# Performance work log

Hardware: AMD Instinct MI355X
Metric: run time of the kernel (lower is better)

## Reference

```python
import jax, jax.numpy as jnp
import numpy as np

GAMMA = 2.0
ALPHA = 0.25
NEG_TH = 0.4
POS_TH = 0.5
NUM_CLASSES = 80
STRIDES = [8, 16, 32, 64, 128]
IMG_H, IMG_W = 800, 1024
LEVEL_HW = [(100, 128), (50, 64), (25, 32), (13, 16), (7, 8)]


def _base_anchors(stride):
    # standard RetinaNet: octave_base_scale=4, 3 scales/octave, ratios 0.5/1/2
    scales = 4.0 * stride * np.array([2 ** 0, 2 ** (1.0 / 3), 2 ** (2.0 / 3)])
    ratios = np.array([0.5, 1.0, 2.0])
    h_r = np.sqrt(ratios)
    w_r = 1.0 / h_r
    ws = (w_r[:, None] * scales[None, :]).reshape(-1)
    hs = (h_r[:, None] * scales[None, :]).reshape(-1)
    return np.stack([-ws / 2, -hs / 2, ws / 2, hs / 2], axis=1)  # [9,4]


def build_anchors():
    out = []
    for (h, w), s in zip(LEVEL_HW, STRIDES):
        base = _base_anchors(s)
        xs = (np.arange(w) + 0.5) * s
        ys = (np.arange(h) + 0.5) * s
        cx, cy = np.meshgrid(xs, ys)  # [h,w]
        ctr = np.stack([cx, cy, cx, cy], axis=-1)  # [h,w,4]
        a = ctr[:, :, None, :] + base[None, None, :, :]  # [h,w,9,4] anchor-fastest
        out.append(a.reshape(-1, 4))
    return jnp.asarray(np.concatenate(out, axis=0), dtype=jnp.float32)  # [A,4]


def _iou(gt, an):  # [G,4],[A,4] -> [G,A]
    lt = jnp.maximum(gt[:, None, :2], an[None, :, :2])
    rb = jnp.minimum(gt[:, None, 2:], an[None, :, 2:])
    wh = jnp.clip(rb - lt, 0.0)
    inter = wh[..., 0] * wh[..., 1]
    area_g = (gt[:, 2] - gt[:, 0]) * (gt[:, 3] - gt[:, 1])
    area_a = (an[:, 2] - an[:, 0]) * (an[:, 3] - an[:, 1])
    return inter / (area_g[:, None] + area_a[None, :] - inter + 1e-6)


def _encode(an, gt):  # delta encoding, mean=0 std=1
    aw = an[:, 2] - an[:, 0]
    ah = an[:, 3] - an[:, 1]
    ax = (an[:, 0] + an[:, 2]) * 0.5
    ay = (an[:, 1] + an[:, 3]) * 0.5
    gw = gt[:, 2] - gt[:, 0]
    gh = gt[:, 3] - gt[:, 1]
    gx = (gt[:, 0] + gt[:, 2]) * 0.5
    gy = (gt[:, 1] + gt[:, 3]) * 0.5
    return jnp.stack([(gx - ax) / aw, (gy - ay) / ah, jnp.log(gw / aw), jnp.log(gh / ah)], axis=1)


def _per_image(logits, regp, gtb, gtl, anchors):
    G = gtb.shape[0]
    iou = _iou(gtb, anchors)  # [G,A]
    max_ov = iou.max(axis=0)
    arg_ov = iou.argmax(axis=0)
    assigned = jnp.where(max_ov < NEG_TH, 0, -1)
    assigned = jnp.where(max_ov >= POS_TH, arg_ov + 1, assigned)
    max_gt = iou.max(axis=1)
    eq = iou == max_gt[:, None]
    any_eq = eq.any(axis=0)
    last_j = (G - 1) - jnp.argmax(eq[::-1], axis=0)
    assigned = jnp.where(any_eq, last_j + 1, assigned)
    pos = assigned > 0
    neg = assigned == 0
    gi = jnp.clip(assigned - 1, 0, G - 1)
    labels = jnp.where(pos, gtl[gi], NUM_CLASSES)  # negatives get label = num_classes
    include = (pos | neg).astype(logits.dtype)  # ignored anchors contribute 0
    # focal loss
    p = jnp.clip(jax.nn.sigmoid(logits), 1e-6, 1.0 - 1e-6)
    cr = jnp.arange(NUM_CLASSES)[None, :]
    t = labels[:, None]
    term1 = (1.0 - p) ** GAMMA * jnp.log(p)
    term2 = p ** GAMMA * jnp.log(1.0 - p)
    per = -(t == cr).astype(p.dtype) * term1 * ALPHA - ((t != cr) & (t >= 0)).astype(p.dtype) * term2 * (1.0 - ALPHA)
    cls_sum = (per.sum(axis=1) * include).sum()
    # smooth-free L1 on positives
    reg_t = _encode(anchors, gtb[gi])
    reg_sum = (jnp.abs(regp - reg_t).sum(axis=1) * pos.astype(regp.dtype)).sum()
    return cls_sum, reg_sum, pos.sum()


def _flatten_levels(levels, c):
    n = levels[0].shape[0]
    return jnp.concatenate([p.transpose(0, 2, 3, 1).reshape(n, -1, c) for p in levels], axis=1)


def reference(cls_p0, cls_p1, cls_p2, cls_p3, cls_p4, reg_p0, reg_p1, reg_p2, reg_p3, reg_p4, gt_bboxes, gt_labels):
    anchors = build_anchors()
    cls = _flatten_levels([cls_p0, cls_p1, cls_p2, cls_p3, cls_p4], NUM_CLASSES)  # [N,A,80]
    reg = _flatten_levels([reg_p0, reg_p1, reg_p2, reg_p3, reg_p4], 4)  # [N,A,4]
    cls_s, reg_s, npos = jax.vmap(lambda l, r, b, t: _per_image(l, r, b, t, anchors))(cls, reg, gt_bboxes, gt_labels)
    num_pos = jnp.maximum(npos.sum(), 1).astype(cls.dtype)
    return (cls_s.sum() / num_pos, reg_s.sum() / num_pos)


def setup_inputs() -> dict:
    key = jax.random.key(0)
    ks = jax.random.split(key, 16)
    N, G = 2, 32
    d = {}
    for i, (h, w) in enumerate(LEVEL_HW):
        d[f"cls_p{i}"] = jax.random.normal(ks[i], (N, 9 * NUM_CLASSES, h, w), jnp.float32)
        d[f"reg_p{i}"] = jax.random.normal(ks[5 + i], (N, 9 * 4, h, w), jnp.float32)
    cx = jax.random.uniform(ks[10], (N, G), minval=50.0, maxval=IMG_W - 50.0)
    cy = jax.random.uniform(ks[11], (N, G), minval=50.0, maxval=IMG_H - 50.0)
    bw = jax.random.uniform(ks[12], (N, G), minval=32.0, maxval=300.0)
    bh = jax.random.uniform(ks[13], (N, G), minval=32.0, maxval=300.0)
    x1 = jnp.clip(cx - bw / 2, 0.0, IMG_W - 2.0)
    y1 = jnp.clip(cy - bh / 2, 0.0, IMG_H - 2.0)
    x2 = jnp.clip(cx + bw / 2, x1 + 1.0, float(IMG_W))
    y2 = jnp.clip(cy + bh / 2, y1 + 1.0, float(IMG_H))
    d["gt_bboxes"] = jnp.stack([x1, y1, x2, y2], axis=-1)
    d["gt_labels"] = jax.random.randint(ks[14], (N, G), 0, NUM_CLASSES)
    return d
```

## Files before the change

kernel.cpp:

```cpp
#include <hip/hip_runtime.h>
#include <stdint.h>

namespace {
constexpr int A_TOTAL = 153576;
constexpr int NG      = 32;
constexpr int NIMG    = 2;
constexpr int NCLS    = 80;
constexpr int NBLK_CLS = 2430;

constexpr size_t WS_CLS0  = 0;
constexpr size_t WS_REG   = 2048;
constexpr size_t WS_NPOS  = 4096;
constexpr size_t WS_MAXGT = 6144;
constexpr size_t WS_LABEL = 6656;
constexpr size_t WS_ZERO  = 6656;
}

__device__ __attribute__((noinline)) float4 anchor_box(int idx) {
    int base, lw, stride;
    if      (idx < 115200) { base = 0;      lw = 7; stride = 8;   }
    else if (idx < 144000) { base = 115200; lw = 6; stride = 16;  }
    else if (idx < 151200) { base = 144000; lw = 5; stride = 32;  }
    else if (idx < 153072) { base = 151200; lw = 4; stride = 64;  }
    else                   { base = 153072; lw = 3; stride = 128; }
    int s    = idx - base;
    int cell = s / 9;
    int a    = s - cell * 9;
    int y    = cell >> lw;
    int x    = cell - (y << lw);
    int r    = a / 3;
    int k    = a - r * 3;
    double c3 = (k == 0) ? 1.0 : ((k == 1) ? 1.2599210498948731648 : 1.5874010519681994748);
    double hr = (r == 0) ? 0.70710678118654752440 : ((r == 1) ? 1.0 : 1.4142135623730950488);
    double scale = 4.0 * (double)stride * c3;
    double wr  = 1.0 / hr;
    double wsz = wr * scale;
    double hsz = hr * scale;
    double cx  = ((double)x + 0.5) * (double)stride;
    double cy  = ((double)y + 0.5) * (double)stride;
    float4 out;
    out.x = (float)(cx - wsz / 2.0);
    out.y = (float)(cy - hsz / 2.0);
    out.z = (float)(cx + wsz / 2.0);
    out.w = (float)(cy + hsz / 2.0);
    return out;
}

__device__ __forceinline__ float iou_fn(float4 an, float4 g) {
#pragma clang fp contract(off)
    float ltx = fmaxf(g.x, an.x), lty = fmaxf(g.y, an.y);
    float rbx = fminf(g.z, an.z), rby = fminf(g.w, an.w);
    float w = fmaxf(rbx - ltx, 0.f), h = fmaxf(rby - lty, 0.f);
    float inter = w * h;
    float ag = (g.z - g.x) * (g.w - g.y);
    float aa = (an.z - an.x) * (an.w - an.y);
    return inter / (ag + aa - inter + 1e-6f);
}

__global__ __launch_bounds__(256)
void kmaxgt(const float* __restrict__ gtb, unsigned* __restrict__ maxgt) {
    int n   = blockIdx.y;
    int tid = threadIdx.x;
    int anchor = blockIdx.x * 128 + (tid >> 1);
    int half   = tid & 1;
    __shared__ float4   g_s[NG];
    __shared__ unsigned smax[NG];
    if (tid < NG) {
        g_s[tid]  = ((const float4*)gtb)[n * NG + tid];
        smax[tid] = 0u;
    }
    __syncthreads();
    bool  valid = anchor < A_TOTAL;
    float4 an = anchor_box(valid ? anchor : 0);
    int lane = tid & 63;
    for (int jj = 0; jj < 16; ++jj) {
        int j = half * 16 + jj;
        float iou = valid ? iou_fn(an, g_s[j]) : 0.f;
        for (int off = 2; off <= 32; off <<= 1)
            iou = fmaxf(iou, __shfl_xor(iou, off));
        if (lane < 2) atomicMax(&smax[j], __float_as_uint(iou));
    }
    __syncthreads();
    if (tid < NG) atomicMax(&maxgt[n * NG + tid], smax[tid]);
}

__global__ __launch_bounds__(256)
void kassign(const float* __restrict__ gtb, const int* __restrict__ gtl,
             const float* __restrict__ maxgt, uint8_t* __restrict__ labels,
             const float* __restrict__ r0, const float* __restrict__ r1,
             const float* __restrict__ r2, const float* __restrict__ r3,
             const float* __restrict__ r4,
             char* __restrict__ ws) {
    int n   = blockIdx.y;
    int tid = threadIdx.x;
    int anchor = blockIdx.x * 128 + (tid >> 1);
    int half   = tid & 1;
    __shared__ float4 g_s[NG];
    __shared__ float  mg_s[NG];
    __shared__ int    gl_s[NG];
    if (tid < NG) {
        g_s[tid]  = ((const float4*)gtb)[n * NG + tid];
        mg_s[tid] = maxgt[n * NG + tid];
        gl_s[tid] = gtl[n * NG + tid];
    }
    __syncthreads();
    bool  valid = anchor < A_TOTAL;
    float4 an = anchor_box(valid ? anchor : 0);
    float best = -1.f; int arg = 0; int last = -1;
    for (int jj = 0; jj < 16; ++jj) {
        int j = half * 16 + jj;
        float iou = iou_fn(an, g_s[j]);
        if (iou > best) { best = iou; arg = j; }
        if (iou == mg_s[j]) last = j;
    }
    float ob = __shfl_xor(best, 1);
    int   oa = __shfl_xor(arg, 1);
    int   ol = __shfl_xor(last, 1);
    if (ob > best) { best = ob; arg = oa; }
    if (ol > last) last = ol;
    int assigned = -1;
    if (best < 0.4f)  assigned = 0;
    if (best >= 0.5f) assigned = arg + 1;
    if (last >= 0)    assigned = last + 1;

    float rsum = 0.f; bool pos = false;
    if (valid && half == 0) {
        int base, HW; const float* rp;
        if      (anchor < 115200) { base = 0;      HW = 12800; rp = r0; }
        else if (anchor < 144000) { base = 115200; HW = 3200;  rp = r1; }
        else if (anchor < 151200) { base = 144000; HW = 800;   rp = r2; }
        else if (anchor < 153072) { base = 151200; HW = 208;   rp = r3; }
        else                      { base = 153072; HW = 56;    rp = r4; }
        int s = anchor - base;
        int cell = s / 9; int a = s - cell * 9;

        uint8_t lab;
        if (assigned > 0) {
            pos = true;
            int gi = assigned - 1;
            lab = (uint8_t)gl_s[gi];
            float aw = an.z - an.x, ah = an.w - an.y;
            float ax = (an.x + an.z) * 0.5f, ay = (an.y + an.w) * 0.5f;
            float4 g = g_s[gi];
            float gw = g.z - g.x, gh = g.w - g.y;
            float gx = (g.x + g.z) * 0.5f, gy = (g.y + g.w) * 0.5f;
            float t0 = (gx - ax) / aw, t1 = (gy - ay) / ah;
            float t2 = __logf(gw / aw), t3 = __logf(gh / ah);
            long off = (long)(n * 36 + a * 4) * HW + cell;
            float p0 = rp[off], p1 = rp[off + HW], p2 = rp[off + 2 * HW], p3 = rp[off + 3 * HW];
            rsum = fabsf(p0 - t0) + fabsf(p1 - t1) + fabsf(p2 - t2) + fabsf(p3 - t3);
        } else {
            lab = (assigned == 0) ? (uint8_t)NCLS : (uint8_t)255;
        }
        labels[n * A_TOTAL + base + a * HW + cell] = lab;
    }
    for (int off = 32; off; off >>= 1) rsum += __shfl_xor(rsum, off);
    unsigned long long bal = __ballot(pos);
    __shared__ float pr[4];
    __shared__ int   pn[4];
    int wid = tid >> 6;
    if ((tid & 63) == 0) { pr[wid] = rsum; pn[wid] = __popcll(bal); }
    __syncthreads();
    if (tid == 0) {
        float s = pr[0] + pr[1] + pr[2] + pr[3];
        int   c = pn[0] + pn[1] + pn[2] + pn[3];
        size_t slot = (size_t)(blockIdx.x & 7) * 256;
        atomicAdd((double*)(ws + WS_REG  + slot), (double)s);
        atomicAdd((int*)   (ws + WS_NPOS + slot), c);
    }
}

__device__ __forceinline__ float focal(float z, int c, int lab) {
    float e   = __expf(z);
    float u   = 1.f + e;
    float inv = __builtin_amdgcn_rcpf(u);
    float L   = __logf(u);
    float p   = e * inv;
    float t2  = 0.75f * (p * p) * L;
    float t1  = 0.25f * (inv * inv) * (L - z);
    float r   = (c == lab) ? t1 : t2;
    return (lab == 255) ? 0.f : r;
}

template <int HW, int BASE, int BPL>
__device__ float cls_level(const float* __restrict__ cp,
                           const uint8_t* __restrict__ labels, int rel, int lane) {
    int slab  = rel / (BPL * 4);
    int rem   = rel - slab * (BPL * 4);
    int chunk = rem >> 2;
    int cq    = rem & 3;
    int n = slab / 9, a = slab - 9 * n;
    int cell = chunk * 128 + 2 * lane;
    if (cell >= HW) return 0.f;
    int lb = n * A_TOTAL + BASE + a * HW + cell;
    int lab0 = labels[lb], lab1 = labels[lb + 1];
    const float* p = cp + (size_t)(n * 720 + a * 80 + cq * 20) * HW + cell;
    int cbase = cq * 20;
    float acc = 0.f;
#pragma unroll 10
    for (int c = 0; c < 20; ++c, p += HW) {
        float2 z = *(const float2*)p;
        acc += focal(z.x, cbase + c, lab0);
        acc += focal(z.y, cbase + c, lab1);
    }
    return acc;
}

__global__ __launch_bounds__(256)
void kcls(const float* __restrict__ c0, const float* __restrict__ c1,
          const float* __restrict__ c2, const float* __restrict__ c3,
          const float* __restrict__ c4,
          const uint8_t* __restrict__ labels, char* __restrict__ ws) {
    int lane = (int)threadIdx.x & 63;
    int b    = blockIdx.x * 4 + ((int)threadIdx.x >> 6);
    float v;
    if      (b < 7200) v = cls_level<12800, 0,      100>(c0, labels, b, lane);
    else if (b < 9000) v = cls_level<3200,  115200, 25 >(c1, labels, b - 7200, lane);
    else if (b < 9504) v = cls_level<800,   144000, 7  >(c2, labels, b - 9000, lane);
    else if (b < 9648) v = cls_level<208,   151200, 2  >(c3, labels, b - 9504, lane);
    else               v = cls_level<56,    153072, 1  >(c4, labels, b - 9648, lane);
    for (int off = 32; off; off >>= 1) v += __shfl_xor(v, off);
    if (lane == 0)
        atomicAdd((double*)(ws + WS_CLS0 + (size_t)(b & 7) * 256), (double)v);
}

__global__ void kfinal(const char* __restrict__ ws, float* __restrict__ out) {
    double cls = 0.0, reg = 0.0;
    int np = 0;
    for (int i = 0; i < 8; ++i) {
        cls += *(const double*)(ws + WS_CLS0 + (size_t)i * 256);
        reg += *(const double*)(ws + WS_REG  + (size_t)i * 256);
        np  += *(const int*)   (ws + WS_NPOS + (size_t)i * 256);
    }
    float denom = (float)(np > 1 ? np : 1);
    out[0] = (float)cls / denom;
    out[1] = (float)reg / denom;
}

extern "C" void kernel_launch(void* const* d_in, const int* in_sizes, int n_in,
                              void* d_out, int out_size, void* d_ws, size_t ws_size,
                              hipStream_t stream) {
    static const int HWs[5] = {12800, 3200, 800, 208, 56};
    const float* cls_p[5] = {nullptr, nullptr, nullptr, nullptr, nullptr};
    const float* reg_p[5] = {nullptr, nullptr, nullptr, nullptr, nullptr};
    const float* gtb = nullptr;
    const int*   gtl = nullptr;
    for (int i = 0; i < n_in; ++i) {
        int sz = in_sizes[i];
        if (sz == NIMG * NG * 4) { gtb = (const float*)d_in[i]; continue; }
        if (sz == NIMG * NG)     { gtl = (const int*)d_in[i];   continue; }
        for (int l = 0; l < 5; ++l) {
            if (sz == NIMG * 9 * NCLS * HWs[l]) { cls_p[l] = (const float*)d_in[i]; break; }
            if (sz == NIMG * 9 * 4 * HWs[l])    { reg_p[l] = (const float*)d_in[i]; break; }
        }
    }
    float* out = (float*)d_out;

    char* ws = (char*)d_ws;
    hipMemsetAsync(d_ws, 0, WS_ZERO, stream);
    unsigned* maxgt_u = (unsigned*)(ws + WS_MAXGT);
    float*    maxgt_f = (float*)(ws + WS_MAXGT);
    uint8_t*  labels  = (uint8_t*)(ws + WS_LABEL);

    dim3 gAB((A_TOTAL + 127) / 128, NIMG);
    kmaxgt<<<gAB, 256, 0, stream>>>(gtb, maxgt_u);
    kassign<<<gAB, 256, 0, stream>>>(gtb, gtl, maxgt_f, labels,
                                     reg_p[0], reg_p[1], reg_p[2], reg_p[3], reg_p[4],
                                     ws);
    kcls<<<NBLK_CLS, 256, 0, stream>>>(cls_p[0], cls_p[1], cls_p[2], cls_p[3], cls_p[4],
                                       labels, ws);
    kfinal<<<1, 1, 0, stream>>>(ws, out);
}
```

Baseline: 195.0 us.

## Precompute anchors and restructure max-IoU kernel with register accumulation and padded atomics

Adds a kernel that materializes all anchor boxes once into workspace, so the max-IoU pass no longer recomputes them with double-precision math. The max-IoU kernel becomes a persistent grid-stride loop: each thread keeps 32 running maxima in registers and does a single wave reduction and atomic per GT at the end. This replaces the earlier per-GT shuffle reduction and atomics on every anchor. The global per-GT maxima are also padded to separate cache lines to reduce atomic contention. In exchange it adds an extra launch, roughly 2.4 MB of anchor writes and reads, and register pressure from the 32-entry array.

After: 186.9 us. 4.1% less time.

```diff
diff --git a/kernel.cpp b/kernel.cpp
--- a/kernel.cpp
+++ b/kernel.cpp
@@ -7,13 +7,15 @@
 constexpr int NIMG    = 2;
 constexpr int NCLS    = 80;
 constexpr int NBLK_CLS = 2430;
+constexpr int NBLK_MG  = 256;
 
 constexpr size_t WS_CLS0  = 0;
 constexpr size_t WS_REG   = 2048;
 constexpr size_t WS_NPOS  = 4096;
 constexpr size_t WS_MAXGT = 6144;
-constexpr size_t WS_LABEL = 6656;
-constexpr size_t WS_ZERO  = 6656;
+constexpr size_t WS_ZERO  = 10240;
+constexpr size_t WS_ANCH  = 12288;
+constexpr size_t WS_LABEL = WS_ANCH + (size_t)A_TOTAL * 16;
 }
 
 __device__ __attribute__((noinline)) float4 anchor_box(int idx) {
@@ -58,11 +60,16 @@
 }
 
 __global__ __launch_bounds__(256)
-void kmaxgt(const float* __restrict__ gtb, unsigned* __restrict__ maxgt) {
+void kanchor(float4* __restrict__ anch) {
+    int idx = blockIdx.x * 256 + (int)threadIdx.x;
+    if (idx < A_TOTAL) anch[idx] = anchor_box(idx);
+}
+
+__global__ __launch_bounds__(256)
+void kmaxgt(const float* __restrict__ gtb, const float4* __restrict__ anch,
+            unsigned* __restrict__ maxgt_p) {
     int n   = blockIdx.y;
     int tid = threadIdx.x;
-    int anchor = blockIdx.x * 128 + (tid >> 1);
-    int half   = tid & 1;
     __shared__ float4   g_s[NG];
     __shared__ unsigned smax[NG];
     if (tid < NG) {
@@ -70,23 +77,30 @@
         smax[tid] = 0u;
     }
     __syncthreads();
-    bool  valid = anchor < A_TOTAL;
-    float4 an = anchor_box(valid ? anchor : 0);
-    int lane = tid & 63;
-    for (int jj = 0; jj < 16; ++jj) {
-        int j = half * 16 + jj;
-        float iou = valid ? iou_fn(an, g_s[j]) : 0.f;
-        for (int off = 2; off <= 32; off <<= 1)
-            iou = fmaxf(iou, __shfl_xor(iou, off));
-        if (lane < 2) atomicMax(&smax[j], __float_as_uint(iou));
-    }
-    __syncthreads();
-    if (tid < NG) atomicMax(&maxgt[n * NG + tid], smax[tid]);
+    float rmax[NG];
+#pragma unroll
+    for (int j = 0; j < NG; ++j) rmax[j] = 0.f;
+    int stride = NBLK_MG * 256;
+    for (int a = blockIdx.x * 256 + tid; a < A_TOTAL; a += stride) {
+        float4 an = anch[a];
+#pragma unroll
+        for (int j = 0; j < NG; ++j)
+            rmax[j] = fmaxf(rmax[j], iou_fn(an, g_s[j]));
+    }
+#pragma unroll
+    for (int j = 0; j < NG; ++j) {
+        float v = rmax[j];
+        for (int off = 1; off <= 32; off <<= 1)
+            v = fmaxf(v, __shfl_xor(v, off));
+        if ((tid & 63) == 0) atomicMax(&smax[j], __float_as_uint(v));
+    }
+    __syncthreads();
+    if (tid < NG) atomicMax(&maxgt_p[(n * NG + tid) * 16], smax[tid]);
 }
 
 __global__ __launch_bounds__(256)
 void kassign(const float* __restrict__ gtb, const int* __restrict__ gtl,
-             const float* __restrict__ maxgt, uint8_t* __restrict__ labels,
+             const unsigned* __restrict__ maxgt_p, uint8_t* __restrict__ labels,
              const float* __restrict__ r0, const float* __restrict__ r1,
              const float* __restrict__ r2, const float* __restrict__ r3,
              const float* __restrict__ r4,
@@ -100,7 +114,7 @@
     __shared__ int    gl_s[NG];
     if (tid < NG) {
         g_s[tid]  = ((const float4*)gtb)[n * NG + tid];
-        mg_s[tid] = maxgt[n * NG + tid];
+        mg_s[tid] = __uint_as_float(maxgt_p[(n * NG + tid) * 16]);
         gl_s[tid] = gtl[n * NG + tid];
     }
     __syncthreads();
@@ -258,15 +272,17 @@
 
     char* ws = (char*)d_ws;
     hipMemsetAsync(d_ws, 0, WS_ZERO, stream);
-    unsigned* maxgt_u = (unsigned*)(ws + WS_MAXGT);
-    float*    maxgt_f = (float*)(ws + WS_MAXGT);
+    unsigned* maxgt_p = (unsigned*)(ws + WS_MAXGT);
+    float4*   anch    = (float4*)(ws + WS_ANCH);
     uint8_t*  labels  = (uint8_t*)(ws + WS_LABEL);
 
-    dim3 gAB((A_TOTAL + 127) / 128, NIMG);
-    kmaxgt<<<gAB, 256, 0, stream>>>(gtb, maxgt_u);
-    kassign<<<gAB, 256, 0, stream>>>(gtb, gtl, maxgt_f, labels,
-                                     reg_p[0], reg_p[1], reg_p[2], reg_p[3], reg_p[4],
-                                     ws);
+    kanchor<<<(A_TOTAL + 255) / 256, 256, 0, stream>>>(anch);
+    dim3 gA(NBLK_MG, NIMG);
+    kmaxgt<<<gA, 256, 0, stream>>>(gtb, anch, maxgt_p);
+    dim3 gB((A_TOTAL + 127) / 128, NIMG);
+    kassign<<<gB, 256, 0, stream>>>(gtb, gtl, maxgt_p, labels,
+                                    reg_p[0], reg_p[1], reg_p[2], reg_p[3], reg_p[4],
+                                    ws);
     kcls<<<NBLK_CLS, 256, 0, stream>>>(cls_p[0], cls_p[1], cls_p[2], cls_p[3], cls_p[4],
                                        labels, ws);
     kfinal<<<1, 1, 0, stream>>>(ws, out);
```
